# Kernel tuning notes

Measured on AMD Instinct MI355X. Metric: run time of the kernel, lower is better.

Reference implementation:

```python
import jax, jax.numpy as jnp
import numpy as np

B, I, O, T, L = 16, 512, 512, 256, 4096
EPS = 1e-8


def setup_inputs() -> dict:
    key = jax.random.key(0)
    ks = jax.random.split(key, 10)
    def lin_w(k, out_d, in_d):  # kaiming-uniform-ish init like torch Linear
        bound = 1.0 / np.sqrt(in_d)
        return jax.random.uniform(k, (out_d, in_d), jnp.float32, -bound, bound)
    return {
        "x": jax.random.normal(ks[0], (B, I, L), jnp.float32),
        "t": jax.random.normal(ks[1], (B, T), jnp.float32),
        "weight": lin_w(ks[2], O, I),            # base conv weight [O, I]
        "W1": lin_w(ks[3], T, T), "b1": jnp.zeros((T,), jnp.float32),
        "W2": lin_w(ks[4], T, T), "b2": jnp.zeros((T,), jnp.float32),
        "W3": lin_w(ks[5], I, T), "b3": jnp.zeros((I,), jnp.float32),
    }


def reference(x, t, weight, W1, b1, W2, b2, W3, b3):
    # mod MLP: Linear -> SiLU -> Linear -> SiLU -> Linear
    h = jax.nn.silu(t @ W1.T + b1)
    h = jax.nn.silu(h @ W2.T + b2)
    s = h @ W3.T + b3 + 1.0                    # [B, I] modulation scales
    bw = weight[None, :, :] * s[:, None, :]    # [B, O, I]
    demod = jax.lax.rsqrt(jnp.sum(bw * bw, axis=2) + EPS)  # [B, O]
    bw = bw * demod[:, :, None]                # demodulated per-sample weights
    # grouped 1x1 conv (groups=B) == batched pointwise contraction
    return jnp.einsum('boi,bil->bol', bw, x)   # [B, O, L]
```

## Files before the change

### kernel.cpp

```cpp
#include <hip/hip_runtime.h>
#include <hip/hip_bf16.h>

typedef float f4v __attribute__((ext_vector_type(4)));
typedef float f32x4 __attribute__((ext_vector_type(4)));
typedef __bf16 bf16x8 __attribute__((ext_vector_type(8)));

#define GLDS16(gsrc, ldst)                                                  \
  __builtin_amdgcn_global_load_lds(                                         \
      (const __attribute__((address_space(1))) unsigned int*)(gsrc),        \
      (__attribute__((address_space(3))) unsigned int*)(ldst), 16, 0, 0)

__device__ __forceinline__ unsigned pack2bf(float lo, float hi) {
  unsigned short ua = __builtin_bit_cast(unsigned short, (__bf16)lo);
  unsigned short ub = __builtin_bit_cast(unsigned short, (__bf16)hi);
  return (unsigned)ua | ((unsigned)ub << 16);
}

__global__ __launch_bounds__(256) void mlp_kernel(
    const float* __restrict__ t,
    const float* __restrict__ W1, const float* __restrict__ b1,
    const float* __restrict__ W2, const float* __restrict__ b2,
    const float* __restrict__ W3, const float* __restrict__ b3,
    float* __restrict__ s_out) {
  __shared__ float tt[256];
  __shared__ float hh[256];
  const int b = blockIdx.x;
  const int tid = threadIdx.x;
  tt[tid] = t[b * 256 + tid];
  __syncthreads();
  float acc = b1[tid];
  {
    const f4v* wrow = (const f4v*)(W1 + tid * 256);
    #pragma unroll 16
    for (int k = 0; k < 64; ++k) {
      f4v wv = wrow[k];
      acc += wv[0] * tt[4 * k] + wv[1] * tt[4 * k + 1] +
             wv[2] * tt[4 * k + 2] + wv[3] * tt[4 * k + 3];
    }
  }
  float h = acc / (1.0f + expf(-acc));
  __syncthreads();
  hh[tid] = h;
  __syncthreads();
  acc = b2[tid];
  {
    const f4v* wrow = (const f4v*)(W2 + tid * 256);
    #pragma unroll 16
    for (int k = 0; k < 64; ++k) {
      f4v wv = wrow[k];
      acc += wv[0] * hh[4 * k] + wv[1] * hh[4 * k + 1] +
             wv[2] * hh[4 * k + 2] + wv[3] * hh[4 * k + 3];
    }
  }
  h = acc / (1.0f + expf(-acc));
  __syncthreads();
  tt[tid] = h;
  __syncthreads();
  #pragma unroll
  for (int rep = 0; rep < 2; ++rep) {
    const int o = rep * 256 + tid;
    float a3 = b3[o];
    const f4v* wrow = (const f4v*)(W3 + o * 256);
    #pragma unroll 16
    for (int k = 0; k < 64; ++k) {
      f4v wv = wrow[k];
      a3 += wv[0] * tt[4 * k] + wv[1] * tt[4 * k + 1] +
            wv[2] * tt[4 * k + 2] + wv[3] * tt[4 * k + 3];
    }
    s_out[b * 512 + o] = a3 + 1.0f;
  }
}

__global__ __launch_bounds__(256) void modw_kernel(
    const float* __restrict__ weight, const float* __restrict__ s_in,
    unsigned short* __restrict__ bwq) {
  const int tid = threadIdx.x;
  const int wid = (blockIdx.x << 2) | (tid >> 6);
  const int b = wid >> 9;
  const int o = wid & 511;
  const int lane = tid & 63;
  const f4v* wp = (const f4v*)(weight + o * 512 + lane * 8);
  const f4v* sp = (const f4v*)(s_in + b * 512 + lane * 8);
  f4v w0 = wp[0], w1 = wp[1];
  f4v s0 = sp[0], s1 = sp[1];
  float p[8];
  p[0] = w0[0] * s0[0]; p[1] = w0[1] * s0[1];
  p[2] = w0[2] * s0[2]; p[3] = w0[3] * s0[3];
  p[4] = w1[0] * s1[0]; p[5] = w1[1] * s1[1];
  p[6] = w1[2] * s1[2]; p[7] = w1[3] * s1[3];
  float ss = 0.0f;
  #pragma unroll
  for (int i = 0; i < 8; ++i) ss += p[i] * p[i];
  #pragma unroll
  for (int off = 32; off; off >>= 1) ss += __shfl_xor(ss, off);
  const float d = rsqrtf(ss + 1e-8f);
  uint4 outw;
  outw.x = pack2bf(p[0] * d, p[1] * d);
  outw.y = pack2bf(p[2] * d, p[3] * d);
  outw.z = pack2bf(p[4] * d, p[5] * d);
  outw.w = pack2bf(p[6] * d, p[7] * d);
  *(uint4*)(bwq + ((size_t)(b * 512 + o)) * 512 + lane * 8) = outw;
}

__global__ __launch_bounds__(256) void gemm_kernel(
    const float* __restrict__ x, const unsigned short* __restrict__ bwq,
    float* __restrict__ out) {
  __shared__ __align__(16) unsigned short AsBuf[3][128 * 32];
  __shared__ __align__(16) unsigned short BsBuf[2][128 * 32];

  const int bid = blockIdx.x;
  const int swz = ((bid & 7) << 8) | (bid >> 3);
  const int mt = swz & 3;
  const int nt = (swz >> 2) & 31;
  const int bb = swz >> 7;

  const int tid = threadIdx.x;
  const int lane = tid & 63;
  const int wv = tid >> 6;
  const int wr = wv >> 1, wc = wv & 1;

  const unsigned short* abase = bwq + ((size_t)(bb * 512 + mt * 128)) * 512;
  const float* xbase = x + ((size_t)bb * 512) * 4096 + nt * 128;

  const int pq = tid >> 5;
  const int lc = tid & 31;
  const float* xp = xbase + (size_t)(pq * 4) * 4096 + lc * 4;
  const int sw_w = (lc & 3) << 4;

  const int g0 = tid, g1 = 256 + tid;
  const unsigned short* asrc0 = abase + (g0 >> 2) * 512 + (g0 & 3) * 8;
  const unsigned short* asrc1 = abase + (g1 >> 2) * 512 + (g1 & 3) * 8;
  const int aoff0 = g0 * 8;
  const int aoff1 = g1 * 8;

  const int arow = wr * 64 + (lane & 15);
  const int kgo = (lane >> 4) * 8;
  const int nrow0 = wc * 64 + (lane & 15);
  const int sb = (nrow0 >> 2) & 3;
  const int bByte = nrow0 * 64 + (((lane >> 4) ^ sb) << 4);

  f32x4 acc[4][4] = {};

  f4v xa0, xa1, xa2, xa3, xb0, xb1, xb2, xb3;

  unsigned short* pA0 = &AsBuf[0][0];
  unsigned short* pA1 = &AsBuf[1][0];
  unsigned short* pA2 = &AsBuf[2][0];
  char* bs0 = (char*)&BsBuf[0][0];
  char* bs1 = (char*)&BsBuf[1][0];

#define LOADX(R0, R1, R2, R3, STEP)                                         \
  do {                                                                      \
    const float* _p = xp + (size_t)((STEP) * 32) * 4096;                    \
    R0 = *(const f4v*)(_p);                                                 \
    R1 = *(const f4v*)(_p + 4096);                                          \
    R2 = *(const f4v*)(_p + 8192);                                          \
    R3 = *(const f4v*)(_p + 12288);                                         \
  } while (0)

#define STAGEA(STEP, PDST)                                                  \
  do {                                                                      \
    GLDS16(asrc0 + (STEP) * 32, (PDST) + aoff0);                            \
    GLDS16(asrc1 + (STEP) * 32, (PDST) + aoff1);                            \
  } while (0)

#define PACKB(R0, R1, R2, R3, BSP)                                          \
  do {                                                                      \
    _Pragma("unroll")                                                       \
    for (int j = 0; j < 4; ++j) {                                           \
      uint2 val;                                                            \
      val.x = pack2bf(R0[j], R1[j]);                                        \
      val.y = pack2bf(R2[j], R3[j]);                                        \
      const int n = (lc << 2) + j;                                          \
      *(uint2*)((BSP) + n * 64 + ((pq * 8) ^ sw_w)) = val;                  \
    }                                                                       \
  } while (0)

#define BAR()                                                               \
  do {                                                                      \
    asm volatile("s_waitcnt lgkmcnt(0)" ::: "memory");                      \
    __builtin_amdgcn_s_barrier();                                           \
    __builtin_amdgcn_sched_barrier(0);                                      \
  } while (0)

#define COMPUTE(PA, BSP)                                                    \
  do {                                                                      \
    const unsigned short* ab = (PA);                                        \
    bf16x8 a0 = *(const bf16x8*)(ab + arow * 32 + kgo);                     \
    bf16x8 a1 = *(const bf16x8*)(ab + arow * 32 + 512 + kgo);               \
    bf16x8 a2 = *(const bf16x8*)(ab + arow * 32 + 1024 + kgo);              \
    bf16x8 a3 = *(const bf16x8*)(ab + arow * 32 + 1536 + kgo);              \
    bf16x8 bf0 = *(const bf16x8*)((BSP) + bByte);                           \
    bf16x8 bf1 = *(const bf16x8*)((BSP) + bByte + 1024);                    \
    bf16x8 bf2 = *(const bf16x8*)((BSP) + bByte + 2048);                    \
    bf16x8 bf3 = *(const bf16x8*)((BSP) + bByte + 3072);                    \
    acc[0][0] = __builtin_amdgcn_mfma_f32_16x16x32_bf16(a0, bf0, acc[0][0], 0, 0, 0); \
    acc[0][1] = __builtin_amdgcn_mfma_f32_16x16x32_bf16(a0, bf1, acc[0][1], 0, 0, 0); \
    acc[0][2] = __builtin_amdgcn_mfma_f32_16x16x32_bf16(a0, bf2, acc[0][2], 0, 0, 0); \
    acc[0][3] = __builtin_amdgcn_mfma_f32_16x16x32_bf16(a0, bf3, acc[0][3], 0, 0, 0); \
    acc[1][0] = __builtin_amdgcn_mfma_f32_16x16x32_bf16(a1, bf0, acc[1][0], 0, 0, 0); \
    acc[1][1] = __builtin_amdgcn_mfma_f32_16x16x32_bf16(a1, bf1, acc[1][1], 0, 0, 0); \
    acc[1][2] = __builtin_amdgcn_mfma_f32_16x16x32_bf16(a1, bf2, acc[1][2], 0, 0, 0); \
    acc[1][3] = __builtin_amdgcn_mfma_f32_16x16x32_bf16(a1, bf3, acc[1][3], 0, 0, 0); \
    acc[2][0] = __builtin_amdgcn_mfma_f32_16x16x32_bf16(a2, bf0, acc[2][0], 0, 0, 0); \
    acc[2][1] = __builtin_amdgcn_mfma_f32_16x16x32_bf16(a2, bf1, acc[2][1], 0, 0, 0); \
    acc[2][2] = __builtin_amdgcn_mfma_f32_16x16x32_bf16(a2, bf2, acc[2][2], 0, 0, 0); \
    acc[2][3] = __builtin_amdgcn_mfma_f32_16x16x32_bf16(a2, bf3, acc[2][3], 0, 0, 0); \
    acc[3][0] = __builtin_amdgcn_mfma_f32_16x16x32_bf16(a3, bf0, acc[3][0], 0, 0, 0); \
    acc[3][1] = __builtin_amdgcn_mfma_f32_16x16x32_bf16(a3, bf1, acc[3][1], 0, 0, 0); \
    acc[3][2] = __builtin_amdgcn_mfma_f32_16x16x32_bf16(a3, bf2, acc[3][2], 0, 0, 0); \
    acc[3][3] = __builtin_amdgcn_mfma_f32_16x16x32_bf16(a3, bf3, acc[3][3], 0, 0, 0); \
  } while (0)

#define ROT()                                                               \
  do { unsigned short* _t = pA0; pA0 = pA1; pA1 = pA2; pA2 = _t; } while (0)

  STAGEA(0, pA0);
  LOADX(xa0, xa1, xa2, xa3, 0);
  STAGEA(1, pA1);
  LOADX(xb0, xb1, xb2, xb3, 1);

  for (int it2 = 0; it2 < 7; ++it2) {
    const int it = it2 * 2;
    PACKB(xa0, xa1, xa2, xa3, bs0);
    STAGEA(it + 2, pA2);
    LOADX(xa0, xa1, xa2, xa3, it + 2);
    BAR();
    COMPUTE(pA0, bs0);
    ROT();
    PACKB(xb0, xb1, xb2, xb3, bs1);
    STAGEA(it + 3, pA2);
    LOADX(xb0, xb1, xb2, xb3, it + 3);
    BAR();
    COMPUTE(pA0, bs1);
    ROT();
  }
  PACKB(xa0, xa1, xa2, xa3, bs0);
  BAR();
  COMPUTE(pA0, bs0);
  ROT();
  PACKB(xb0, xb1, xb2, xb3, bs1);
  BAR();
  COMPUTE(pA0, bs1);

  const size_t ob =
      ((size_t)(bb * 512 + mt * 128 + wr * 64 + ((lane >> 4) << 2))) * 4096 +
      nt * 128 + wc * 64 + (lane & 15);
  #pragma unroll
  for (int mi = 0; mi < 4; ++mi)
    #pragma unroll
    for (int ni = 0; ni < 4; ++ni)
      #pragma unroll
      for (int jj = 0; jj < 4; ++jj)
        out[ob + (size_t)(mi * 16 + jj) * 4096 + ni * 16] = acc[mi][ni][jj];

#undef LOADX
#undef STAGEA
#undef PACKB
#undef BAR
#undef COMPUTE
#undef ROT
}

extern "C" void kernel_launch(void* const* d_in, const int* in_sizes, int n_in,
                              void* d_out, int out_size, void* d_ws, size_t ws_size,
                              hipStream_t stream) {
  const float* x      = (const float*)d_in[0];
  const float* t      = (const float*)d_in[1];
  const float* weight = (const float*)d_in[2];
  const float* W1     = (const float*)d_in[3];
  const float* b1     = (const float*)d_in[4];
  const float* W2     = (const float*)d_in[5];
  const float* b2     = (const float*)d_in[6];
  const float* W3     = (const float*)d_in[7];
  const float* b3     = (const float*)d_in[8];
  float* out = (float*)d_out;

  float* s_ws = (float*)d_ws;
  unsigned short* bwq = (unsigned short*)((char*)d_ws + 32 * 1024);

  mlp_kernel<<<16, 256, 0, stream>>>(t, W1, b1, W2, b2, W3, b3, s_ws);
  modw_kernel<<<2048, 256, 0, stream>>>(weight, s_ws, bwq);
  gemm_kernel<<<2048, 256, 0, stream>>>(x, bwq, out);
}
```

Before: 127.9 us.

## Deepen GEMM prefetch pipeline to four stages and switch to XOR-swizzled k-major LDS layout

The GEMM now keeps four k-steps of x in registers and A tiles in a five-buffer LDS ring, where before it held two steps and three buffers. More global loads are in flight to hide HBM latency. The LDS layout for both operands changes to k-quarter-major with an XOR row swizzle, and the read offsets are precomputed, to avoid bank conflicts. The cost is extra VGPRs for 16 more float4 prefetch registers and more LDS, which may reduce occupancy.

```diff
diff --git a/kernel.cpp b/kernel.cpp
--- a/kernel.cpp
+++ b/kernel.cpp
@@ -105,8 +105,8 @@
 __global__ __launch_bounds__(256) void gemm_kernel(
     const float* __restrict__ x, const unsigned short* __restrict__ bwq,
     float* __restrict__ out) {
-  __shared__ __align__(16) unsigned short AsBuf[3][128 * 32];
-  __shared__ __align__(16) unsigned short BsBuf[2][128 * 32];
+  __shared__ __align__(16) unsigned short AsBuf[5][4096];
+  __shared__ __align__(16) unsigned short BsBuf[2][4096];
 
   const int bid = blockIdx.x;
   const int swz = ((bid & 7) << 8) | (bid >> 3);
@@ -125,43 +125,59 @@
   const int pq = tid >> 5;
   const int lc = tid & 31;
   const float* xp = xbase + (size_t)(pq * 4) * 4096 + lc * 4;
-  const int sw_w = (lc & 3) << 4;
-
-  const int g0 = tid, g1 = 256 + tid;
-  const unsigned short* asrc0 = abase + (g0 >> 2) * 512 + (g0 & 3) * 8;
-  const unsigned short* asrc1 = abase + (g1 >> 2) * 512 + (g1 & 3) * 8;
-  const int aoff0 = g0 * 8;
-  const int aoff1 = g1 * 8;
-
-  const int arow = wr * 64 + (lane & 15);
-  const int kgo = (lane >> 4) * 8;
-  const int nrow0 = wc * 64 + (lane & 15);
-  const int sb = (nrow0 >> 2) & 3;
-  const int bByte = nrow0 * 64 + (((lane >> 4) ^ sb) << 4);
+
+  const int s0 = tid, s1 = 256 + tid;
+  const int kq0 = s0 >> 7, mp0 = s0 & 127;
+  const int kq1 = s1 >> 7, mp1 = s1 & 127;
+  const int m0 = mp0 ^ ((mp0 >> 3) & 7);
+  const int m1 = mp1 ^ ((mp1 >> 3) & 7);
+  const unsigned short* asrc0 = abase + m0 * 512 + kq0 * 8;
+  const unsigned short* asrc1 = abase + m1 * 512 + kq1 * 8;
+  const int aoff0 = s0 * 8;
+  const int aoff1 = s1 * 8;
+
+  int bw_off[4];
+  #pragma unroll
+  for (int j = 0; j < 4; ++j) {
+    const int n = lc * 4 + j;
+    bw_off[j] = (pq >> 1) * 2048 + (n ^ ((n >> 3) & 7)) * 16 + (pq & 1) * 8;
+  }
+
+  const int kqL = lane >> 4;
+  const int rL = lane & 15;
+  int aro[4], bro[4];
+  #pragma unroll
+  for (int i = 0; i < 4; ++i) {
+    const int m = wr * 64 + i * 16 + rL;
+    aro[i] = kqL * 2048 + (m ^ ((m >> 3) & 7)) * 16;
+    const int n = wc * 64 + i * 16 + rL;
+    bro[i] = kqL * 2048 + (n ^ ((n >> 3) & 7)) * 16;
+  }
 
   f32x4 acc[4][4] = {};
-
   f4v xa0, xa1, xa2, xa3, xb0, xb1, xb2, xb3;
+  f4v xc0, xc1, xc2, xc3, xd0, xd1, xd2, xd3;
 
   unsigned short* pA0 = &AsBuf[0][0];
   unsigned short* pA1 = &AsBuf[1][0];
   unsigned short* pA2 = &AsBuf[2][0];
+  unsigned short* pA3 = &AsBuf[3][0];
+  unsigned short* pA4 = &AsBuf[4][0];
   char* bs0 = (char*)&BsBuf[0][0];
   char* bs1 = (char*)&BsBuf[1][0];
 
-#define LOADX(R0, R1, R2, R3, STEP)                                         \
-  do {                                                                      \
-    const float* _p = xp + (size_t)((STEP) * 32) * 4096;                    \
-    R0 = *(const f4v*)(_p);                                                 \
-    R1 = *(const f4v*)(_p + 4096);                                          \
-    R2 = *(const f4v*)(_p + 8192);                                          \
-    R3 = *(const f4v*)(_p + 12288);                                         \
-  } while (0)
-
-#define STAGEA(STEP, PDST)                                                  \
-  do {                                                                      \
-    GLDS16(asrc0 + (STEP) * 32, (PDST) + aoff0);                            \
-    GLDS16(asrc1 + (STEP) * 32, (PDST) + aoff1);                            \
+#define LOADXP(R0, R1, R2, R3, P)                                           \
+  do {                                                                      \
+    R0 = *(const f4v*)(P);                                                  \
+    R1 = *(const f4v*)((P) + 4096);                                         \
+    R2 = *(const f4v*)((P) + 8192);                                         \
+    R3 = *(const f4v*)((P) + 12288);                                        \
+  } while (0)
+
+#define STAGEA(KOFF, PDST)                                                  \
+  do {                                                                      \
+    GLDS16(asrc0 + (KOFF), (PDST) + aoff0);                                 \
+    GLDS16(asrc1 + (KOFF), (PDST) + aoff1);                                 \
   } while (0)
 
 #define PACKB(R0, R1, R2, R3, BSP)                                          \
@@ -171,11 +187,11 @@
       uint2 val;                                                            \
       val.x = pack2bf(R0[j], R1[j]);                                        \
       val.y = pack2bf(R2[j], R3[j]);                                        \
-      const int n = (lc << 2) + j;                                          \
-      *(uint2*)((BSP) + n * 64 + ((pq * 8) ^ sw_w)) = val;                  \
+      *(uint2*)((BSP) + bw_off[j]) = val;                                   \
     }                                                                       \
   } while (0)
 
+#define FENCE() asm volatile("" ::: "memory")
 #define BAR()                                                               \
   do {                                                                      \
     asm volatile("s_waitcnt lgkmcnt(0)" ::: "memory");                      \
@@ -185,15 +201,15 @@
 
 #define COMPUTE(PA, BSP)                                                    \
   do {                                                                      \
-    const unsigned short* ab = (PA);                                        \
-    bf16x8 a0 = *(const bf16x8*)(ab + arow * 32 + kgo);                     \
-    bf16x8 a1 = *(const bf16x8*)(ab + arow * 32 + 512 + kgo);               \
-    bf16x8 a2 = *(const bf16x8*)(ab + arow * 32 + 1024 + kgo);              \
-    bf16x8 a3 = *(const bf16x8*)(ab + arow * 32 + 1536 + kgo);              \
-    bf16x8 bf0 = *(const bf16x8*)((BSP) + bByte);                           \
-    bf16x8 bf1 = *(const bf16x8*)((BSP) + bByte + 1024);                    \
-    bf16x8 bf2 = *(const bf16x8*)((BSP) + bByte + 2048);                    \
-    bf16x8 bf3 = *(const bf16x8*)((BSP) + bByte + 3072);                    \
+    const char* ab = (const char*)(PA);                                     \
+    bf16x8 a0 = *(const bf16x8*)(ab + aro[0]);                              \
+    bf16x8 a1 = *(const bf16x8*)(ab + aro[1]);                              \
+    bf16x8 a2 = *(const bf16x8*)(ab + aro[2]);                              \
+    bf16x8 a3 = *(const bf16x8*)(ab + aro[3]);                              \
+    bf16x8 bf0 = *(const bf16x8*)((BSP) + bro[0]);                          \
+    bf16x8 bf1 = *(const bf16x8*)((BSP) + bro[1]);                          \
+    bf16x8 bf2 = *(const bf16x8*)((BSP) + bro[2]);                          \
+    bf16x8 bf3 = *(const bf16x8*)((BSP) + bro[3]);                          \
     acc[0][0] = __builtin_amdgcn_mfma_f32_16x16x32_bf16(a0, bf0, acc[0][0], 0, 0, 0); \
     acc[0][1] = __builtin_amdgcn_mfma_f32_16x16x32_bf16(a0, bf1, acc[0][1], 0, 0, 0); \
     acc[0][2] = __builtin_amdgcn_mfma_f32_16x16x32_bf16(a0, bf2, acc[0][2], 0, 0, 0); \
@@ -212,36 +228,39 @@
     acc[3][3] = __builtin_amdgcn_mfma_f32_16x16x32_bf16(a3, bf3, acc[3][3], 0, 0, 0); \
   } while (0)
 
-#define ROT()                                                               \
-  do { unsigned short* _t = pA0; pA0 = pA1; pA1 = pA2; pA2 = _t; } while (0)
-
-  STAGEA(0, pA0);
-  LOADX(xa0, xa1, xa2, xa3, 0);
-  STAGEA(1, pA1);
-  LOADX(xb0, xb1, xb2, xb3, 1);
-
-  for (int it2 = 0; it2 < 7; ++it2) {
-    const int it = it2 * 2;
+#define ROT5()                                                              \
+  do {                                                                      \
+    unsigned short* _t = pA0;                                               \
+    pA0 = pA1; pA1 = pA2; pA2 = pA3; pA3 = pA4; pA4 = _t;                   \
+  } while (0)
+
+  const long long XS = 32LL * 4096;
+  STAGEA(0, pA0);   FENCE();  LOADXP(xa0, xa1, xa2, xa3, xp);
+  STAGEA(32, pA1);  FENCE();  LOADXP(xb0, xb1, xb2, xb3, xp + XS);
+  STAGEA(64, pA2);  FENCE();  LOADXP(xc0, xc1, xc2, xc3, xp + 2 * XS);
+  STAGEA(96, pA3);  FENCE();  LOADXP(xd0, xd1, xd2, xd3, xp + 3 * XS);
+
+  const float* xq = xp + 4 * XS;
+  int koff = 128;
+
+  for (int q = 0; q < 4; ++q) {
     PACKB(xa0, xa1, xa2, xa3, bs0);
-    STAGEA(it + 2, pA2);
-    LOADX(xa0, xa1, xa2, xa3, it + 2);
-    BAR();
-    COMPUTE(pA0, bs0);
-    ROT();
+    if (q < 3) { STAGEA(koff, pA4); FENCE();
+                 LOADXP(xa0, xa1, xa2, xa3, xq); xq += XS; koff += 32; }
+    BAR(); COMPUTE(pA0, bs0); ROT5();
     PACKB(xb0, xb1, xb2, xb3, bs1);
-    STAGEA(it + 3, pA2);
-    LOADX(xb0, xb1, xb2, xb3, it + 3);
-    BAR();
-    COMPUTE(pA0, bs1);
-    ROT();
-  }
-  PACKB(xa0, xa1, xa2, xa3, bs0);
-  BAR();
-  COMPUTE(pA0, bs0);
-  ROT();
-  PACKB(xb0, xb1, xb2, xb3, bs1);
-  BAR();
-  COMPUTE(pA0, bs1);
+    if (q < 3) { STAGEA(koff, pA4); FENCE();
+                 LOADXP(xb0, xb1, xb2, xb3, xq); xq += XS; koff += 32; }
+    BAR(); COMPUTE(pA0, bs1); ROT5();
+    PACKB(xc0, xc1, xc2, xc3, bs0);
+    if (q < 3) { STAGEA(koff, pA4); FENCE();
+                 LOADXP(xc0, xc1, xc2, xc3, xq); xq += XS; koff += 32; }
+    BAR(); COMPUTE(pA0, bs0); ROT5();
+    PACKB(xd0, xd1, xd2, xd3, bs1);
+    if (q < 3) { STAGEA(koff, pA4); FENCE();
+                 LOADXP(xd0, xd1, xd2, xd3, xq); xq += XS; koff += 32; }
+    BAR(); COMPUTE(pA0, bs1); ROT5();
+  }
 
   const size_t ob =
       ((size_t)(bb * 512 + mt * 128 + wr * 64 + ((lane >> 4) << 2))) * 4096 +
@@ -254,12 +273,13 @@
       for (int jj = 0; jj < 4; ++jj)
         out[ob + (size_t)(mi * 16 + jj) * 4096 + ni * 16] = acc[mi][ni][jj];
 
-#undef LOADX
+#undef LOADXP
 #undef STAGEA
 #undef PACKB
+#undef FENCE
 #undef BAR
 #undef COMPUTE
-#undef ROT
+#undef ROT5
 }
 
 extern "C" void kernel_launch(void* const* d_in, const int* in_sizes, int n_in,
```

Measured after the change: 139.9 us. 1.09x slower.
